# Kernel tuning notes

Measured on AMD Instinct MI355X. Metric: run time of the kernel, lower is better.

Reference implementation:

```python
import jax, jax.numpy as jnp
import numpy as np

B, NNODE, D = 128, 64, 64          # graphs, nodes per graph, invariant feat dim
N = B * NNODE                      # 8192 nodes
E = B * NNODE * (NNODE - 1)        # 516096 directed edges (fully connected per graph)


def _silu(x):
    return x * jax.nn.sigmoid(x)


def _ln(x, w, b, eps=1e-5):
    mu = jnp.mean(x, axis=-1, keepdims=True)
    var = jnp.var(x, axis=-1, keepdims=True)
    return (x - mu) / jnp.sqrt(var + eps) * w + b


def setup_inputs() -> dict:
    key = jax.random.key(0)
    ks = jax.random.split(key, 12)
    # node -> graph assignment, sorted
    batch = np.repeat(np.arange(B), NNODE)
    # fully-connected directed edges within each graph (i != j)
    idx = np.arange(NNODE)
    s, d = np.meshgrid(idx, idx, indexing='ij')
    m = s != d
    s, d = s[m], d[m]
    off = (np.arange(B) * NNODE)[:, None]
    src = (s[None, :] + off).ravel()
    dst = (d[None, :] + off).ravel()
    E_idx = jnp.asarray(np.stack([src, dst]), dtype=jnp.int32)
    return dict(
        batch=jnp.asarray(batch, jnp.int32),
        X=jax.random.normal(ks[0], (N, 3), jnp.float32),
        H=jax.random.normal(ks[1], (N, D), jnp.float32),
        E_idx=E_idx,
        x_norm_w=jnp.ones((1, 1), jnp.float32),
        q_w1=jax.random.normal(ks[2], (D, D), jnp.float32) * 0.05,
        q_w2=jax.random.normal(ks[3], (D, D), jnp.float32) * 0.05,
        kv_w1=jax.random.normal(ks[4], (D + 1, 2 * D), jnp.float32) * 0.05,
        kv_w2=jax.random.normal(ks[5], (2 * D, 2 * D), jnp.float32) * 0.05,
        qn_w=jnp.ones((D,), jnp.float32), qn_b=jnp.zeros((D,), jnp.float32),
        kn_w=jnp.ones((D,), jnp.float32), kn_b=jnp.zeros((D,), jnp.float32),
        phx_w1=jax.random.normal(ks[6], (D, D), jnp.float32) * 0.05,
        phx_w2=jax.random.normal(ks[7], (D, 1), jnp.float32) * 0.05,
        phh_w1=jax.random.normal(ks[8], (D, D), jnp.float32) * 0.05,
        phh_b1=jnp.zeros((D,), jnp.float32),
        phh_w2=jax.random.normal(ks[9], (D, D), jnp.float32) * 0.05,
        phh_b2=jnp.zeros((D,), jnp.float32),
    )


def reference(batch, X, H, E_idx, x_norm_w, q_w1, q_w2, kv_w1, kv_w2,
              qn_w, qn_b, kn_w, kn_b, phx_w1, phx_w2,
              phh_w1, phh_b1, phh_w2, phh_b2):
    src, dst = E_idx[0], E_idx[1]
    # ---- E3Norm: scale positions by per-graph mean norm ----
    norm = jnp.linalg.norm(X, axis=-1, keepdims=True)                 # [N,1]
    cnt = jax.ops.segment_sum(jnp.ones((N,), X.dtype), batch, num_segments=B)
    mean_norm = jax.ops.segment_sum(norm, batch, num_segments=B) / cnt[:, None]
    Xn = x_norm_w * X / (mean_norm[batch] + 1e-5)                     # [N,3]
    # ---- edge gathers + MLPs ----
    Q = _silu(H[dst] @ q_w1) @ q_w2                                   # [E,D]
    rel = Xn[src] - Xn[dst]                                           # [E,3]
    rel_dist = jnp.sum(rel * rel, axis=-1, keepdims=True)             # [E,1]
    X_rel_norm = rel / (1.0 + jnp.sqrt(rel_dist + 1e-8))
    kv_in = jnp.concatenate([rel_dist, H[src]], axis=-1)              # [E,D+1]
    kv = _silu(kv_in @ kv_w1) @ kv_w2                                 # [E,2D]
    K, V = kv[:, :D], kv[:, D:]
    Q = _ln(Q, qn_w, qn_b)
    K = _ln(K, kn_w, kn_b)
    # ---- scatter softmax over incoming edges of dst ----
    scores = jnp.sum(Q * K, axis=-1) / jnp.sqrt(jnp.asarray(D, X.dtype))  # [E]
    m = jax.ops.segment_max(scores, dst, num_segments=N)
    e = jnp.exp(scores - m[dst])
    s = jax.ops.segment_sum(e, dst, num_segments=N)
    alpha = e / s[dst]                                                # [E]
    att = alpha[:, None] * V                                          # [E,D]
    # ---- scatter-sum aggregations ----
    A = jax.ops.segment_sum(att, dst, num_segments=N)                 # [N,D]
    AH = jax.ops.segment_sum(att * H[dst], dst, num_segments=N)       # [N,D]
    phx = _silu(att @ phx_w1) @ phx_w2                                # [E,1]
    X_out = Xn + jax.ops.segment_sum(X_rel_norm * phx, dst, num_segments=N)
    H_out = H + (_silu((A * AH) @ phh_w1 + phh_b1) @ phh_w2 + phh_b2)
    return X_out, H_out
```

## Files before the change

kernel.cpp:

```cpp
#include <hip/hip_runtime.h>
#include <math.h>

#define NB     128
#define NNODE  64
#define NTOT   8192
#define DIM    64
#define PSTR   136
#define WS72   72

typedef __bf16 bf16x8 __attribute__((ext_vector_type(8)));
typedef float  f32x4  __attribute__((ext_vector_type(4)));

__device__ __forceinline__ float frcp(float x) {
    return __builtin_amdgcn_rcpf(x);
}

__device__ __forceinline__ float silu_f(float x) {
    return x * frcp(1.0f + __expf(-x));
}

__device__ __forceinline__ unsigned short bf16bits(float f) {
    return __builtin_bit_cast(unsigned short, (__bf16)f);
}

__device__ __forceinline__ bf16x8 to_bf16x8(const float* v) {
    bf16x8 o;
    #pragma unroll
    for (int j = 0; j < 8; ++j) o[j] = (__bf16)v[j];
    return o;
}

__device__ __forceinline__ float wsum(float v) {
    #pragma unroll
    for (int m = 1; m < 64; m <<= 1) v += __shfl_xor(v, m, 64);
    return v;
}

__global__ __launch_bounds__(256) void k0_prep(
        const float* __restrict__ kvw2, const float* __restrict__ phxw1,
        const float* __restrict__ X, const float* __restrict__ xw,
        const float* __restrict__ qw1, const float* __restrict__ qw2,
        const float* __restrict__ kvw1,
        const float* __restrict__ phh1, const float* __restrict__ phh2,
        unsigned short* __restrict__ w2x, float* __restrict__ Xn4,
        unsigned short* __restrict__ qw1T, unsigned short* __restrict__ qw2T,
        unsigned short* __restrict__ kvw1T,
        unsigned short* __restrict__ phh1T, unsigned short* __restrict__ phh2T) {
    const int k = blockIdx.x;
    const int T = threadIdx.x;
    if (T < 128) {
        w2x[T*PSTR + k] = bf16bits(kvw2[k*128 + T]);
    } else if (T < 192) {
        const int n2 = T - 128;
        float acc = 0.f;
        #pragma unroll 8
        for (int j = 0; j < 64; ++j)
            acc += kvw2[k*128 + 64 + j] * phxw1[j*64 + n2];
        w2x[(128 + n2)*PSTR + k] = bf16bits(acc);
    } else {
        const int L = T - 192;
        const int n = k*64 + L;
        const float x0 = X[n*3+0], x1 = X[n*3+1], x2 = X[n*3+2];
        const float nm = sqrtf(x0*x0 + x1*x1 + x2*x2);
        const float mean = wsum(nm) * (1.0f/64.0f);
        const float sc = xw[0] * frcp(mean + 1e-5f);
        float4 o; o.x = x0*sc; o.y = x1*sc; o.z = x2*sc; o.w = 0.f;
        *(float4*)&Xn4[n*4] = o;
    }
    if (k < 64) {
        if (T < 128) kvw1T[T*WS72 + k] = bf16bits(kvw1[(1+k)*128 + T]);
    } else {
        const int kk = k - 64;
        if (T < 64)       qw1T[T*WS72 + kk]        = bf16bits(qw1[kk*64 + T]);
        else if (T < 128) qw2T[(T-64)*WS72 + kk]   = bf16bits(qw2[kk*64 + (T-64)]);
        else if (T < 192) phh1T[(T-128)*WS72 + kk] = bf16bits(phh1[kk*64 + (T-128)]);
        else              phh2T[(T-192)*WS72 + kk] = bf16bits(phh2[kk*64 + (T-192)]);
    }
}

__global__ __launch_bounds__(128) void k2_node(
        const float* __restrict__ H,
        const unsigned short* __restrict__ qw1T,
        const unsigned short* __restrict__ qw2T,
        const unsigned short* __restrict__ kvw1T,
        const float* __restrict__ qnw, const float* __restrict__ qnb,
        float* __restrict__ Qn, unsigned short* __restrict__ Ptb) {
    const int nb = blockIdx.x * 32;
    const int T = threadIdx.x, w = T >> 6, L = T & 63;
    const int q = L >> 4, m = L & 15;
    __shared__ __align__(16) unsigned short zb[32*WS72];

    bf16x8 hf[2];
    #pragma unroll
    for (int ks = 0; ks < 2; ++ks) {
        float v[8];
        *(float4*)&v[0] = *(const float4*)&H[(size_t)(nb + w*16 + m)*64 + ks*32 + q*8];
        *(float4*)&v[4] = *(const float4*)&H[(size_t)(nb + w*16 + m)*64 + ks*32 + q*8 + 4];
        hf[ks] = to_bf16x8(v);
    }

    f32x4 acc[4];
    #pragma unroll
    for (int ct = 0; ct < 4; ++ct) acc[ct] = (f32x4){0.f,0.f,0.f,0.f};
    #pragma unroll
    for (int ks = 0; ks < 2; ++ks)
        #pragma unroll
        for (int ct = 0; ct < 4; ++ct) {
            const bf16x8 b = *(const bf16x8*)&qw1T[(ct*16 + m)*WS72 + ks*32 + q*8];
            acc[ct] = __builtin_amdgcn_mfma_f32_16x16x32_bf16(hf[ks], b, acc[ct], 0, 0, 0);
        }
    #pragma unroll
    for (int ct = 0; ct < 4; ++ct)
        #pragma unroll
        for (int r = 0; r < 4; ++r)
            zb[(w*16 + q*4 + r)*WS72 + ct*16 + m] = bf16bits(silu_f(acc[ct][r]));
    __syncthreads();

    bf16x8 zf[2];
    #pragma unroll
    for (int ks = 0; ks < 2; ++ks)
        zf[ks] = *(const bf16x8*)&zb[(w*16 + m)*WS72 + ks*32 + q*8];
    #pragma unroll
    for (int ct = 0; ct < 4; ++ct) acc[ct] = (f32x4){0.f,0.f,0.f,0.f};
    #pragma unroll
    for (int ks = 0; ks < 2; ++ks)
        #pragma unroll
        for (int ct = 0; ct < 4; ++ct) {
            const bf16x8 b = *(const bf16x8*)&qw2T[(ct*16 + m)*WS72 + ks*32 + q*8];
            acc[ct] = __builtin_amdgcn_mfma_f32_16x16x32_bf16(zf[ks], b, acc[ct], 0, 0, 0);
        }
    float qnwv[4], qnbv[4];
    #pragma unroll
    for (int ct = 0; ct < 4; ++ct) { qnwv[ct] = qnw[ct*16+m]; qnbv[ct] = qnb[ct*16+m]; }
    #pragma unroll
    for (int r = 0; r < 4; ++r) {
        float s1 = 0.f, s2 = 0.f;
        #pragma unroll
        for (int ct = 0; ct < 4; ++ct) {
            const float z = acc[ct][r];
            s1 += z; s2 = fmaf(z, z, s2);
        }
        #pragma unroll
        for (int sh = 1; sh < 16; sh <<= 1) {
            s1 += __shfl_xor(s1, sh, 64);
            s2 += __shfl_xor(s2, sh, 64);
        }
        const float mu = s1 * (1.0f/64.0f);
        const float rstd = rsqrtf(s2 * (1.0f/64.0f) - mu*mu + 1e-5f);
        const int row = nb + w*16 + q*4 + r;
        #pragma unroll
        for (int ct = 0; ct < 4; ++ct)
            Qn[(size_t)row*64 + ct*16 + m] = (acc[ct][r] - mu)*rstd*qnwv[ct] + qnbv[ct];
    }

    #pragma unroll
    for (int ph = 0; ph < 2; ++ph) {
        #pragma unroll
        for (int ct = 0; ct < 4; ++ct) acc[ct] = (f32x4){0.f,0.f,0.f,0.f};
        #pragma unroll
        for (int ks = 0; ks < 2; ++ks)
            #pragma unroll
            for (int ct = 0; ct < 4; ++ct) {
                const bf16x8 b = *(const bf16x8*)&kvw1T[(ph*64 + ct*16 + m)*WS72 + ks*32 + q*8];
                acc[ct] = __builtin_amdgcn_mfma_f32_16x16x32_bf16(hf[ks], b, acc[ct], 0, 0, 0);
            }
        #pragma unroll
        for (int ct = 0; ct < 4; ++ct)
            #pragma unroll
            for (int r = 0; r < 4; ++r)
                Ptb[(size_t)(nb + w*16 + q*4 + r)*PSTR + ph*64 + ct*16 + m]
                    = bf16bits(acc[ct][r]);
    }
}

__global__ __launch_bounds__(512, 4) void k3_edge(
        const float* __restrict__ Xn4, const float* __restrict__ Qn,
        const unsigned short* __restrict__ Ptb,
        const unsigned short* __restrict__ w2x,
        const float* __restrict__ kvw1,
        const float* __restrict__ knw, const float* __restrict__ knb,
        const float* __restrict__ pxw2,
        float* __restrict__ Abuf, float* __restrict__ Xout) {
    const int bid = blockIdx.x;
    const int g = bid >> 2, dgrp = bid & 3;
    const int T = threadIdx.x, w = T >> 6, L = T & 63;
    const int q = L >> 4, m = L & 15;
    const int pair = w >> 1, half = w & 1;

    __shared__ __align__(16) unsigned short sw2[192*PSTR];
    __shared__ __align__(16) float sXn[64][4];
    __shared__ __align__(16) float sQn[16][64];
    __shared__ __align__(16) float sxr[8][32][4];
    __shared__ float w0s[128];
    __shared__ float knws[64], knbs[64], pxs[64];
    __shared__ float sred[4][2][2];
    __shared__ float sA[4][64];
    __shared__ float sX[4][4];

    {
        const uint4* s1 = (const uint4*)w2x;
        uint4* d1 = (uint4*)sw2;
        for (int idx = T; idx < 192*PSTR/8; idx += 512) d1[idx] = s1[idx];
        const float* qsrc = Qn + ((size_t)g*64 + dgrp*16)*64;
        for (int idx = T; idx < 1024; idx += 512)
            sQn[idx >> 6][idx & 63] = qsrc[idx];
        if (T < 64) *(float4*)&sXn[T][0] = *(const float4*)&Xn4[(g*64 + T)*4];
        if (T < 128) w0s[T] = kvw1[T];
        if (T < 64)            knws[T]       = knw[T];
        else if (T < 128)      knbs[T - 64]  = knb[T - 64];
        else if (T < 192)      pxs[T - 128]  = pxw2[T - 128];
    }
    __syncthreads();

    const unsigned short* PtG = Ptb + (size_t)g*64*PSTR;

    #pragma unroll 1
    for (int i = 0; i < 4; ++i) {
        const int dql = i*4 + pair;
        const int dl  = dgrp*16 + dql;
        const int d   = g*64 + dl;

        if (L < 32) {
            const int row = half*32 + L;
            const float4 xs  = *(const float4*)&sXn[row][0];
            const float4 xdv = *(const float4*)&sXn[dl][0];
            const float r0 = xs.x - xdv.x, r1 = xs.y - xdv.y, r2 = xs.z - xdv.z;
            const float rd = r0*r0 + r1*r1 + r2*r2;
            const float inv = frcp(1.0f + sqrtf(rd + 1e-8f));
            float4 o; o.x = r0*inv; o.y = r1*inv; o.z = r2*inv; o.w = rd;
            *(float4*)&sxr[w][L][0] = o;
        }

        bf16x8 af[2][4];
        float rdv[2];
        #pragma unroll
        for (int rt = 0; rt < 2; ++rt) rdv[rt] = sxr[w][rt*16 + m][3];
        #pragma unroll
        for (int ks = 0; ks < 4; ++ks) {
            float w0v[8];
            *(float4*)&w0v[0] = *(const float4*)&w0s[ks*32 + q*8];
            *(float4*)&w0v[4] = *(const float4*)&w0s[ks*32 + q*8 + 4];
            #pragma unroll
            for (int rt = 0; rt < 2; ++rt) {
                const int row = half*32 + rt*16 + m;
                const bf16x8 pb = *(const bf16x8*)&PtG[(size_t)row*PSTR + ks*32 + q*8];
                bf16x8 o;
                #pragma unroll
                for (int j = 0; j < 8; ++j) {
                    const float pf = (float)pb[j];
                    o[j] = (__bf16)silu_f(fmaf(rdv[rt], w0v[j], pf));
                }
                af[rt][ks] = o;
            }
        }

        f32x4 acc[4][2];

        #pragma unroll
        for (int ct = 0; ct < 4; ++ct)
            #pragma unroll
            for (int rt = 0; rt < 2; ++rt)
                acc[ct][rt] = (f32x4){0.f, 0.f, 0.f, 0.f};
        #pragma unroll
        for (int ks = 0; ks < 4; ++ks)
            #pragma unroll
            for (int ct = 0; ct < 4; ++ct) {
                const bf16x8 b = *(const bf16x8*)&sw2[(ct*16 + m)*PSTR + ks*32 + q*8];
                #pragma unroll
                for (int rt = 0; rt < 2; ++rt)
                    acc[ct][rt] = __builtin_amdgcn_mfma_f32_16x16x32_bf16(
                                      af[rt][ks], b, acc[ct][rt], 0, 0, 0);
            }

        float qdw[4], Sqdw = 0.f, Sqdb = 0.f;
        #pragma unroll
        for (int ct = 0; ct < 4; ++ct) {
            const float qd = sQn[dql][ct*16 + m];
            qdw[ct] = qd * knws[ct*16 + m];
            Sqdw += qdw[ct];
            Sqdb += qd * knbs[ct*16 + m];
        }
        #pragma unroll
        for (int sh = 1; sh < 16; sh <<= 1) {
            Sqdw += __shfl_xor(Sqdw, sh, 64);
            Sqdb += __shfl_xor(Sqdb, sh, 64);
        }
        float sc[2][4];
        #pragma unroll
        for (int rt = 0; rt < 2; ++rt)
            #pragma unroll
            for (int r = 0; r < 4; ++r) {
                float s1 = 0.f, s2 = 0.f, skq = 0.f;
                #pragma unroll
                for (int ct = 0; ct < 4; ++ct) {
                    const float kv = acc[ct][rt][r];
                    s1 += kv; s2 = fmaf(kv, kv, s2); skq = fmaf(kv, qdw[ct], skq);
                }
                #pragma unroll
                for (int sh = 1; sh < 16; sh <<= 1) {
                    s1  += __shfl_xor(s1,  sh, 64);
                    s2  += __shfl_xor(s2,  sh, 64);
                    skq += __shfl_xor(skq, sh, 64);
                }
                const float mu = s1 * (1.0f/64.0f);
                const float rstd = rsqrtf(s2 * (1.0f/64.0f) - mu*mu + 1e-5f);
                const float scv = (rstd * (skq - mu*Sqdw) + Sqdb) * 0.125f;
                const int row_g = half*32 + rt*16 + q*4 + r;
                sc[rt][r] = (row_g == dl) ? -1e30f : scv;
            }

        float mx = -1e30f;
        #pragma unroll
        for (int rt = 0; rt < 2; ++rt)
            #pragma unroll
            for (int r = 0; r < 4; ++r) mx = fmaxf(mx, sc[rt][r]);
        mx = fmaxf(mx, __shfl_xor(mx, 16, 64));
        mx = fmaxf(mx, __shfl_xor(mx, 32, 64));
        float al[2][4], S = 0.f;
        #pragma unroll
        for (int rt = 0; rt < 2; ++rt)
            #pragma unroll
            for (int r = 0; r < 4; ++r) {
                al[rt][r] = __expf(sc[rt][r] - mx);
                S += al[rt][r];
            }
        S += __shfl_xor(S, 16, 64);
        S += __shfl_xor(S, 32, 64);
        S *= 0.25f;
        S *= 4.0f;
        if (L == 0) { sred[pair][half][0] = mx; sred[pair][half][1] = S; }
        __syncthreads();
        {
            const float mo = sred[pair][half^1][0];
            const float So = sred[pair][half^1][1];
            const float M  = fmaxf(mx, mo);
            const float es = __expf(mx - M);
            const float eo = __expf(mo - M);
            const float alf = es * frcp(S*es + So*eo);
            #pragma unroll
            for (int rt = 0; rt < 2; ++rt)
                #pragma unroll
                for (int r = 0; r < 4; ++r) al[rt][r] *= alf;
        }

        #pragma unroll
        for (int ct = 0; ct < 4; ++ct)
            #pragma unroll
            for (int rt = 0; rt < 2; ++rt)
                acc[ct][rt] = (f32x4){0.f, 0.f, 0.f, 0.f};
        #pragma unroll
        for (int ks = 0; ks < 4; ++ks)
            #pragma unroll
            for (int ct = 0; ct < 4; ++ct) {
                const bf16x8 b = *(const bf16x8*)&sw2[(64 + ct*16 + m)*PSTR + ks*32 + q*8];
                #pragma unroll
                for (int rt = 0; rt < 2; ++rt)
                    acc[ct][rt] = __builtin_amdgcn_mfma_f32_16x16x32_bf16(
                                      af[rt][ks], b, acc[ct][rt], 0, 0, 0);
            }
        float p[4];
        #pragma unroll
        for (int ct = 0; ct < 4; ++ct) {
            float pv = 0.f;
            #pragma unroll
            for (int rt = 0; rt < 2; ++rt)
                #pragma unroll
                for (int r = 0; r < 4; ++r)
                    pv = fmaf(al[rt][r], acc[ct][rt][r], pv);
            pv += __shfl_xor(pv, 16, 64);
            pv += __shfl_xor(pv, 32, 64);
            p[ct] = pv;
        }
        if (half == 1 && q == 0)
            #pragma unroll
            for (int ct = 0; ct < 4; ++ct) sA[pair][ct*16 + m] = p[ct];
        __syncthreads();
        if (half == 0 && q == 0)
            #pragma unroll
            for (int ct = 0; ct < 4; ++ct)
                Abuf[(size_t)d*64 + ct*16 + m] = p[ct] + sA[pair][ct*16 + m];

        #pragma unroll
        for (int ct = 0; ct < 4; ++ct)
            #pragma unroll
            for (int rt = 0; rt < 2; ++rt)
                acc[ct][rt] = (f32x4){0.f, 0.f, 0.f, 0.f};
        #pragma unroll
        for (int ks = 0; ks < 4; ++ks)
            #pragma unroll
            for (int ct = 0; ct < 4; ++ct) {
                const bf16x8 b = *(const bf16x8*)&sw2[(128 + ct*16 + m)*PSTR + ks*32 + q*8];
                #pragma unroll
                for (int rt = 0; rt < 2; ++rt)
                    acc[ct][rt] = __builtin_amdgcn_mfma_f32_16x16x32_bf16(
                                      af[rt][ks], b, acc[ct][rt], 0, 0, 0);
            }

        float pxc[4];
        #pragma unroll
        for (int ct = 0; ct < 4; ++ct) pxc[ct] = pxs[ct*16 + m];
        float xa0 = 0.f, xa1 = 0.f, xa2 = 0.f;
        #pragma unroll
        for (int rt = 0; rt < 2; ++rt)
            #pragma unroll
            for (int r = 0; r < 4; ++r) {
                float ph = 0.f;
                #pragma unroll
                for (int ct = 0; ct < 4; ++ct)
                    ph = fmaf(silu_f(al[rt][r] * acc[ct][rt][r]), pxc[ct], ph);
                #pragma unroll
                for (int sh = 1; sh < 16; sh <<= 1) ph += __shfl_xor(ph, sh, 64);
                const float4 xr = *(const float4*)&sxr[w][rt*16 + q*4 + r][0];
                xa0 = fmaf(ph, xr.x, xa0);
                xa1 = fmaf(ph, xr.y, xa1);
                xa2 = fmaf(ph, xr.z, xa2);
            }
        xa0 += __shfl_xor(xa0, 16, 64); xa0 += __shfl_xor(xa0, 32, 64);
        xa1 += __shfl_xor(xa1, 16, 64); xa1 += __shfl_xor(xa1, 32, 64);
        xa2 += __shfl_xor(xa2, 16, 64); xa2 += __shfl_xor(xa2, 32, 64);
        if (half == 1 && L == 0) {
            sX[pair][0] = xa0; sX[pair][1] = xa1; sX[pair][2] = xa2;
        }
        __syncthreads();
        if (half == 0 && L == 0) {
            const float4 xdv = *(const float4*)&sXn[dl][0];
            Xout[(size_t)d*3 + 0] = xdv.x + xa0 + sX[pair][0];
            Xout[(size_t)d*3 + 1] = xdv.y + xa1 + sX[pair][1];
            Xout[(size_t)d*3 + 2] = xdv.z + xa2 + sX[pair][2];
        }
    }
}

__global__ __launch_bounds__(128) void k4_hout(
        const float* __restrict__ H, const float* __restrict__ Abuf,
        const unsigned short* __restrict__ phh1T, const float* __restrict__ b1,
        const unsigned short* __restrict__ phh2T, const float* __restrict__ b2,
        float* __restrict__ Hout) {
    const int nb = blockIdx.x * 32;
    const int T = threadIdx.x, w = T >> 6, L = T & 63;
    const int q = L >> 4, m = L & 15;
    __shared__ __align__(16) unsigned short zb[32*WS72];

    bf16x8 uf[2];
    #pragma unroll
    for (int ks = 0; ks < 2; ++ks) {
        const size_t base = (size_t)(nb + w*16 + m)*64 + ks*32 + q*8;
        float a[8], h[8], v[8];
        *(float4*)&a[0] = *(const float4*)&Abuf[base];
        *(float4*)&a[4] = *(const float4*)&Abuf[base + 4];
        *(float4*)&h[0] = *(const float4*)&H[base];
        *(float4*)&h[4] = *(const float4*)&H[base + 4];
        #pragma unroll
        for (int j = 0; j < 8; ++j) v[j] = a[j]*a[j]*h[j];
        uf[ks] = to_bf16x8(v);
    }

    f32x4 acc[4];
    #pragma unroll
    for (int ct = 0; ct < 4; ++ct) acc[ct] = (f32x4){0.f,0.f,0.f,0.f};
    #pragma unroll
    for (int ks = 0; ks < 2; ++ks)
        #pragma unroll
        for (int ct = 0; ct < 4; ++ct) {
            const bf16x8 b = *(const bf16x8*)&phh1T[(ct*16 + m)*WS72 + ks*32 + q*8];
            acc[ct] = __builtin_amdgcn_mfma_f32_16x16x32_bf16(uf[ks], b, acc[ct], 0, 0, 0);
        }
    #pragma unroll
    for (int ct = 0; ct < 4; ++ct) {
        const float bv = b1[ct*16 + m];
        #pragma unroll
        for (int r = 0; r < 4; ++r)
            zb[(w*16 + q*4 + r)*WS72 + ct*16 + m] = bf16bits(silu_f(acc[ct][r] + bv));
    }
    __syncthreads();

    bf16x8 zf[2];
    #pragma unroll
    for (int ks = 0; ks < 2; ++ks)
        zf[ks] = *(const bf16x8*)&zb[(w*16 + m)*WS72 + ks*32 + q*8];
    #pragma unroll
    for (int ct = 0; ct < 4; ++ct) acc[ct] = (f32x4){0.f,0.f,0.f,0.f};
    #pragma unroll
    for (int ks = 0; ks < 2; ++ks)
        #pragma unroll
        for (int ct = 0; ct < 4; ++ct) {
            const bf16x8 b = *(const bf16x8*)&phh2T[(ct*16 + m)*WS72 + ks*32 + q*8];
            acc[ct] = __builtin_amdgcn_mfma_f32_16x16x32_bf16(zf[ks], b, acc[ct], 0, 0, 0);
        }
    #pragma unroll
    for (int ct = 0; ct < 4; ++ct) {
        const float bv = b2[ct*16 + m];
        #pragma unroll
        for (int r = 0; r < 4; ++r) {
            const size_t idx = (size_t)(nb + w*16 + q*4 + r)*64 + ct*16 + m;
            Hout[idx] = H[idx] + acc[ct][r] + bv;
        }
    }
}

extern "C" void kernel_launch(void* const* d_in, const int* in_sizes, int n_in,
                              void* d_out, int out_size, void* d_ws, size_t ws_size,
                              hipStream_t stream) {
    const float* X    = (const float*)d_in[1];
    const float* H    = (const float*)d_in[2];
    const float* xw   = (const float*)d_in[4];
    const float* qw1  = (const float*)d_in[5];
    const float* qw2  = (const float*)d_in[6];
    const float* kvw1 = (const float*)d_in[7];
    const float* kvw2 = (const float*)d_in[8];
    const float* qnw  = (const float*)d_in[9];
    const float* qnb  = (const float*)d_in[10];
    const float* knw  = (const float*)d_in[11];
    const float* knb  = (const float*)d_in[12];
    const float* pxw1 = (const float*)d_in[13];
    const float* pxw2 = (const float*)d_in[14];
    const float* phw1 = (const float*)d_in[15];
    const float* phb1 = (const float*)d_in[16];
    const float* phw2 = (const float*)d_in[17];
    const float* phb2 = (const float*)d_in[18];

    float* out = (float*)d_out;
    char*  ws  = (char*)d_ws;

    size_t off = 0;
    float* Xn4 = (float*)(ws + off);          off += (size_t)NTOT*4*4;
    float* Qn  = (float*)(ws + off);          off += (size_t)NTOT*64*4;
    unsigned short* Ptb = (unsigned short*)(ws + off); off += (size_t)NTOT*PSTR*2;
    float* Ab  = (float*)(ws + off);          off += (size_t)NTOT*64*4;
    unsigned short* w2x   = (unsigned short*)(ws + off); off += (size_t)192*PSTR*2;
    unsigned short* qw1T  = (unsigned short*)(ws + off); off += (size_t)64*WS72*2;
    unsigned short* qw2T  = (unsigned short*)(ws + off); off += (size_t)64*WS72*2;
    unsigned short* kvw1T = (unsigned short*)(ws + off); off += (size_t)128*WS72*2;
    unsigned short* phh1T = (unsigned short*)(ws + off); off += (size_t)64*WS72*2;
    unsigned short* phh2T = (unsigned short*)(ws + off); off += (size_t)64*WS72*2;

    k0_prep<<<128, 256, 0, stream>>>(kvw2, pxw1, X, xw, qw1, qw2, kvw1,
                                     phw1, phw2, w2x, Xn4,
                                     qw1T, qw2T, kvw1T, phh1T, phh2T);
    k2_node<<<256, 128, 0, stream>>>(H, qw1T, qw2T, kvw1T, qnw, qnb, Qn, Ptb);
    k3_edge<<<512, 512, 0, stream>>>(Xn4, Qn, Ptb, w2x, kvw1, knw, knb,
                                     pxw2, Ab, out);
    k4_hout<<<256, 128, 0, stream>>>(H, Ab, phh1T, phb1, phh2T, phb2,
                                     out + NTOT*3);
}
```

Before: 196.7 us.

## Stage node weights in LDS and shrink edge-kernel blocks to 256 threads

The node and output kernels now copy their transposed bf16 weights into shared memory once per block and read MFMA operands from there instead of global memory. This relies on the weight buffers being contiguous in the workspace. The edge kernel drops from 512 to 256 threads per block, with each block handling 8 destinations instead of 16, and the grid doubles to 1024 blocks. It also stages only 128 rows of the combined weight in LDS and reads the remaining phx weight straight from global/L2. This lowers the LDS footprint to allow more resident blocks, at the cost of extra global traffic for those weights and a redundant explicit waitcnt.

Result: faster. 184.9 us (-6.0%).

```diff
diff --git a/kernel.cpp b/kernel.cpp
--- a/kernel.cpp
+++ b/kernel.cpp
@@ -81,14 +81,20 @@
 __global__ __launch_bounds__(128) void k2_node(
         const float* __restrict__ H,
         const unsigned short* __restrict__ qw1T,
-        const unsigned short* __restrict__ qw2T,
-        const unsigned short* __restrict__ kvw1T,
         const float* __restrict__ qnw, const float* __restrict__ qnb,
         float* __restrict__ Qn, unsigned short* __restrict__ Ptb) {
     const int nb = blockIdx.x * 32;
     const int T = threadIdx.x, w = T >> 6, L = T & 63;
     const int q = L >> 4, m = L & 15;
+    __shared__ __align__(16) unsigned short swt[256*WS72];
     __shared__ __align__(16) unsigned short zb[32*WS72];
+
+    {
+        const uint4* s = (const uint4*)qw1T;
+        uint4* d = (uint4*)swt;
+        #pragma unroll
+        for (int it = 0; it < 18; ++it) d[T + 128*it] = s[T + 128*it];
+    }
 
     bf16x8 hf[2];
     #pragma unroll
@@ -98,6 +104,7 @@
         *(float4*)&v[4] = *(const float4*)&H[(size_t)(nb + w*16 + m)*64 + ks*32 + q*8 + 4];
         hf[ks] = to_bf16x8(v);
     }
+    __syncthreads();
 
     f32x4 acc[4];
     #pragma unroll
@@ -106,7 +113,7 @@
     for (int ks = 0; ks < 2; ++ks)
         #pragma unroll
         for (int ct = 0; ct < 4; ++ct) {
-            const bf16x8 b = *(const bf16x8*)&qw1T[(ct*16 + m)*WS72 + ks*32 + q*8];
+            const bf16x8 b = *(const bf16x8*)&swt[(ct*16 + m)*WS72 + ks*32 + q*8];
             acc[ct] = __builtin_amdgcn_mfma_f32_16x16x32_bf16(hf[ks], b, acc[ct], 0, 0, 0);
         }
     #pragma unroll
@@ -126,7 +133,7 @@
     for (int ks = 0; ks < 2; ++ks)
         #pragma unroll
         for (int ct = 0; ct < 4; ++ct) {
-            const bf16x8 b = *(const bf16x8*)&qw2T[(ct*16 + m)*WS72 + ks*32 + q*8];
+            const bf16x8 b = *(const bf16x8*)&swt[(64 + ct*16 + m)*WS72 + ks*32 + q*8];
             acc[ct] = __builtin_amdgcn_mfma_f32_16x16x32_bf16(zf[ks], b, acc[ct], 0, 0, 0);
         }
     float qnwv[4], qnbv[4];
@@ -161,7 +168,7 @@
         for (int ks = 0; ks < 2; ++ks)
             #pragma unroll
             for (int ct = 0; ct < 4; ++ct) {
-                const bf16x8 b = *(const bf16x8*)&kvw1T[(ph*64 + ct*16 + m)*WS72 + ks*32 + q*8];
+                const bf16x8 b = *(const bf16x8*)&swt[(128 + ph*64 + ct*16 + m)*WS72 + ks*32 + q*8];
                 acc[ct] = __builtin_amdgcn_mfma_f32_16x16x32_bf16(hf[ks], b, acc[ct], 0, 0, 0);
             }
         #pragma unroll
@@ -173,7 +180,7 @@
     }
 }
 
-__global__ __launch_bounds__(512, 4) void k3_edge(
+__global__ __launch_bounds__(256, 3) void k3_edge(
         const float* __restrict__ Xn4, const float* __restrict__ Qn,
         const unsigned short* __restrict__ Ptb,
         const unsigned short* __restrict__ w2x,
@@ -182,27 +189,31 @@
         const float* __restrict__ pxw2,
         float* __restrict__ Abuf, float* __restrict__ Xout) {
     const int bid = blockIdx.x;
-    const int g = bid >> 2, dgrp = bid & 3;
+    const int g = bid >> 3, dgrp = bid & 7;
     const int T = threadIdx.x, w = T >> 6, L = T & 63;
     const int q = L >> 4, m = L & 15;
     const int pair = w >> 1, half = w & 1;
 
-    __shared__ __align__(16) unsigned short sw2[192*PSTR];
+    __shared__ __align__(16) unsigned short sw2[128*PSTR];
     __shared__ __align__(16) float sXn[64][4];
-    __shared__ __align__(16) float sQn[16][64];
-    __shared__ __align__(16) float sxr[8][32][4];
+    __shared__ __align__(16) float sQn[8][64];
+    __shared__ __align__(16) float sxr[4][32][4];
     __shared__ float w0s[128];
     __shared__ float knws[64], knbs[64], pxs[64];
-    __shared__ float sred[4][2][2];
-    __shared__ float sA[4][64];
-    __shared__ float sX[4][4];
+    __shared__ float sred[2][2][2];
+    __shared__ float sA[2][64];
+    __shared__ float sX[2][4];
 
     {
         const uint4* s1 = (const uint4*)w2x;
         uint4* d1 = (uint4*)sw2;
-        for (int idx = T; idx < 192*PSTR/8; idx += 512) d1[idx] = s1[idx];
-        const float* qsrc = Qn + ((size_t)g*64 + dgrp*16)*64;
-        for (int idx = T; idx < 1024; idx += 512)
+        #pragma unroll
+        for (int it = 0; it < 9; ++it) {
+            const int idx = T + 256*it;
+            if (idx < 128*PSTR/8) d1[idx] = s1[idx];
+        }
+        const float* qsrc = Qn + ((size_t)g*64 + dgrp*8)*64;
+        for (int idx = T; idx < 512; idx += 256)
             sQn[idx >> 6][idx & 63] = qsrc[idx];
         if (T < 64) *(float4*)&sXn[T][0] = *(const float4*)&Xn4[(g*64 + T)*4];
         if (T < 128) w0s[T] = kvw1[T];
@@ -213,11 +224,12 @@
     __syncthreads();
 
     const unsigned short* PtG = Ptb + (size_t)g*64*PSTR;
+    const unsigned short* Gw  = w2x + 128*PSTR;
 
     #pragma unroll 1
     for (int i = 0; i < 4; ++i) {
-        const int dql = i*4 + pair;
-        const int dl  = dgrp*16 + dql;
+        const int dql = i*2 + pair;
+        const int dl  = dgrp*8 + dql;
         const int d   = g*64 + dl;
 
         if (L < 32) {
@@ -230,6 +242,7 @@
             float4 o; o.x = r0*inv; o.y = r1*inv; o.z = r2*inv; o.w = rd;
             *(float4*)&sxr[w][L][0] = o;
         }
+        asm volatile("s_waitcnt lgkmcnt(0)" ::: "memory");
 
         bf16x8 af[2][4];
         float rdv[2];
@@ -326,8 +339,6 @@
             }
         S += __shfl_xor(S, 16, 64);
         S += __shfl_xor(S, 32, 64);
-        S *= 0.25f;
-        S *= 4.0f;
         if (L == 0) { sred[pair][half][0] = mx; sred[pair][half][1] = S; }
         __syncthreads();
         {
@@ -389,7 +400,7 @@
         for (int ks = 0; ks < 4; ++ks)
             #pragma unroll
             for (int ct = 0; ct < 4; ++ct) {
-                const bf16x8 b = *(const bf16x8*)&sw2[(128 + ct*16 + m)*PSTR + ks*32 + q*8];
+                const bf16x8 b = *(const bf16x8*)&Gw[(size_t)(ct*16 + m)*PSTR + ks*32 + q*8];
                 #pragma unroll
                 for (int rt = 0; rt < 2; ++rt)
                     acc[ct][rt] = __builtin_amdgcn_mfma_f32_16x16x32_bf16(
@@ -434,12 +445,19 @@
 __global__ __launch_bounds__(128) void k4_hout(
         const float* __restrict__ H, const float* __restrict__ Abuf,
         const unsigned short* __restrict__ phh1T, const float* __restrict__ b1,
-        const unsigned short* __restrict__ phh2T, const float* __restrict__ b2,
-        float* __restrict__ Hout) {
+        const float* __restrict__ b2, float* __restrict__ Hout) {
     const int nb = blockIdx.x * 32;
     const int T = threadIdx.x, w = T >> 6, L = T & 63;
     const int q = L >> 4, m = L & 15;
+    __shared__ __align__(16) unsigned short swt[128*WS72];
     __shared__ __align__(16) unsigned short zb[32*WS72];
+
+    {
+        const uint4* s = (const uint4*)phh1T;
+        uint4* d = (uint4*)swt;
+        #pragma unroll
+        for (int it = 0; it < 9; ++it) d[T + 128*it] = s[T + 128*it];
+    }
 
     bf16x8 uf[2];
     #pragma unroll
@@ -454,6 +472,7 @@
         for (int j = 0; j < 8; ++j) v[j] = a[j]*a[j]*h[j];
         uf[ks] = to_bf16x8(v);
     }
+    __syncthreads();
 
     f32x4 acc[4];
     #pragma unroll
@@ -462,7 +481,7 @@
     for (int ks = 0; ks < 2; ++ks)
         #pragma unroll
         for (int ct = 0; ct < 4; ++ct) {
-            const bf16x8 b = *(const bf16x8*)&phh1T[(ct*16 + m)*WS72 + ks*32 + q*8];
+            const bf16x8 b = *(const bf16x8*)&swt[(ct*16 + m)*WS72 + ks*32 + q*8];
             acc[ct] = __builtin_amdgcn_mfma_f32_16x16x32_bf16(uf[ks], b, acc[ct], 0, 0, 0);
         }
     #pragma unroll
@@ -484,7 +503,7 @@
     for (int ks = 0; ks < 2; ++ks)
         #pragma unroll
         for (int ct = 0; ct < 4; ++ct) {
-            const bf16x8 b = *(const bf16x8*)&phh2T[(ct*16 + m)*WS72 + ks*32 + q*8];
+            const bf16x8 b = *(const bf16x8*)&swt[(64 + ct*16 + m)*WS72 + ks*32 + q*8];
             acc[ct] = __builtin_amdgcn_mfma_f32_16x16x32_bf16(zf[ks], b, acc[ct], 0, 0, 0);
         }
     #pragma unroll
@@ -537,9 +556,8 @@
     k0_prep<<<128, 256, 0, stream>>>(kvw2, pxw1, X, xw, qw1, qw2, kvw1,
                                      phw1, phw2, w2x, Xn4,
                                      qw1T, qw2T, kvw1T, phh1T, phh2T);
-    k2_node<<<256, 128, 0, stream>>>(H, qw1T, qw2T, kvw1T, qnw, qnb, Qn, Ptb);
-    k3_edge<<<512, 512, 0, stream>>>(Xn4, Qn, Ptb, w2x, kvw1, knw, knb,
-                                     pxw2, Ab, out);
-    k4_hout<<<256, 128, 0, stream>>>(H, Ab, phh1T, phb1, phh2T, phb2,
-                                     out + NTOT*3);
-}
+    k2_node<<<256, 128, 0, stream>>>(H, qw1T, qnw, qnb, Qn, Ptb);
+    k3_edge<<<1024, 256, 0, stream>>>(Xn4, Qn, Ptb, w2x, kvw1, knw, knb,
+                                      pxw2, Ab, out);
+    k4_hout<<<256, 128, 0, stream>>>(H, Ab, phh1T, phb1, phb2, out + NTOT*3);
+}
```
